# Performance work log

Hardware: AMD Instinct MI355X
Metric: run time of the kernel (lower is better)

Reference implementation:

```python
import jax, jax.numpy as jnp
import numpy as np

N = 8192
F_IN = 256
F_OUT = 64
ALPHA = 0.2  # leaky relu negative slope
MASK_VAL = -9e15


def setup_inputs() -> dict:
    key = jax.random.key(0)
    k1, k2, k3, k4, k5, k6 = jax.random.split(key, 6)
    stdv_lin = 1.0 / np.sqrt(F_IN)
    stdv_a = 1.0 / np.sqrt(2 * F_OUT)
    return {
        "input": jax.random.normal(k1, (N, F_IN), dtype=jnp.float32),
        "adj": jax.random.randint(k2, (N, N), 0, 2, dtype=jnp.int32),
        "W": jax.random.uniform(k3, (F_IN, F_OUT), minval=-stdv_lin, maxval=stdv_lin, dtype=jnp.float32),
        "b_lin": jax.random.uniform(k4, (F_OUT,), minval=-stdv_lin, maxval=stdv_lin, dtype=jnp.float32),
        "a": jax.random.uniform(k5, (2 * F_OUT, 1), minval=-stdv_a, maxval=stdv_a, dtype=jnp.float32),
        "bias": jax.random.uniform(k6, (F_OUT,), minval=-stdv_a, maxval=stdv_a, dtype=jnp.float32),
    }


def reference(input, adj, W, b_lin, a, bias):
    # h = Linear(input): [N, F_OUT]
    h = input @ W + b_lin
    # e[i,j] = leaky_relu(a1 . h_i + a2 . h_j)  (equivalent to the repeat/cat/matmul in torch,
    # without materializing the [N, N, 2*F_OUT] tensor)
    a1 = a[:F_OUT, 0]
    a2 = a[F_OUT:, 0]
    s1 = h @ a1  # [N]
    s2 = h @ a2  # [N]
    e = jax.nn.leaky_relu(s1[:, None] + s2[None, :], negative_slope=ALPHA)  # [N, N]
    attention = jnp.where(adj > 0, e, MASK_VAL)
    attention = jax.nn.softmax(attention, axis=1)
    # dropout is identity in eval mode (training=False)
    output = attention @ h + bias
    return output
```

## Files before the change

### kernel.cpp

```cpp
#include <hip/hip_runtime.h>

#define N 8192
#define FIN 256
#define FOUT 64
#define ALPHA 0.2f
#define LOG2C 3
#define NCHUNK (1 << LOG2C)
#define CLEN (N >> LOG2C)

typedef float f32x4 __attribute__((ext_vector_type(4)));
typedef short s16x8 __attribute__((ext_vector_type(8)));

static __device__ __forceinline__ unsigned short f2bf(float x) {
    unsigned u = __float_as_uint(x);
    u += 0x7fffu + ((u >> 16) & 1u);
    return (unsigned short)(u >> 16);
}

__global__ __launch_bounds__(256) void k_linear(
    const float* __restrict__ input, const float* __restrict__ W,
    const float* __restrict__ b_lin, const float* __restrict__ a,
    unsigned short* __restrict__ hTf, float* __restrict__ s1, float* __restrict__ s2,
    unsigned* __restrict__ s2max_enc)
{
    __shared__ float in_sh[16 * FIN];
    __shared__ float hst[64][17];
    int t = threadIdx.x, w = t >> 6, f = t & 63;
    int b = blockIdx.x;
    int i0 = b * 16;

#pragma unroll
    for (int r = 0; r < 4; r++) {
        int row = w * 4 + r;
        *(float4*)&in_sh[row * FIN + f * 4] =
            *(const float4*)(input + (size_t)(i0 + row) * FIN + f * 4);
    }

    float a1v = a[f], a2v = a[FOUT + f];
    float h[4];
#pragma unroll
    for (int r = 0; r < 4; r++) h[r] = b_lin[f];

    for (int k4 = 0; k4 < FIN / 4; k4++) {
        float wv0 = W[(k4 * 4 + 0) * FOUT + f];
        float wv1 = W[(k4 * 4 + 1) * FOUT + f];
        float wv2 = W[(k4 * 4 + 2) * FOUT + f];
        float wv3 = W[(k4 * 4 + 3) * FOUT + f];
#pragma unroll
        for (int r = 0; r < 4; r++) {
            float4 iv = *(const float4*)&in_sh[(w * 4 + r) * FIN + k4 * 4];
            h[r] = fmaf(iv.x, wv0, h[r]);
            h[r] = fmaf(iv.y, wv1, h[r]);
            h[r] = fmaf(iv.z, wv2, h[r]);
            h[r] = fmaf(iv.w, wv3, h[r]);
        }
    }

    float wmax = -1e30f;
#pragma unroll
    for (int r = 0; r < 4; r++) {
        hst[f][w * 4 + r] = h[r];
        float v1 = h[r] * a1v, v2 = h[r] * a2v;
#pragma unroll
        for (int d = 1; d < 64; d <<= 1) { v1 += __shfl_xor(v1, d); v2 += __shfl_xor(v2, d); }
        wmax = fmaxf(wmax, v2);
        if (f == 0) { s1[i0 + w * 4 + r] = v1; s2[i0 + w * 4 + r] = v2; }
    }
    if (f == 0) {
        unsigned u = __float_as_uint(wmax);
        unsigned key = (u & 0x80000000u) ? ~u : (u | 0x80000000u);
        atomicMax(s2max_enc, key);
    }
    __syncthreads();

    int fo = t >> 2, seg = t & 3;
    unsigned lo = f2bf(hst[fo][seg * 4 + 0]) | ((unsigned)f2bf(hst[fo][seg * 4 + 1]) << 16);
    unsigned hi = f2bf(hst[fo][seg * 4 + 2]) | ((unsigned)f2bf(hst[fo][seg * 4 + 3]) << 16);
    int2 v; v.x = (int)lo; v.y = (int)hi;
    size_t base = (size_t)(b >> 1) * 2048 + (size_t)fo * 32 + (b & 1) * 16 + seg * 4;
    *(int2*)(hTf + base) = v;
}


#define PGEN(AV0, AV1, SVP, AFR) do {                                             \
    float4 sv0 = *(const float4*)(SVP);                                           \
    float4 sv1 = *(const float4*)((SVP) + 4);                                     \
    float p0, p1, p2, p3, p4, p5, p6, p7;                                         \
    { float u = s1c + sv0.x; float g = fmaxf(u, fmaf(0.2f, u, c2)); p0 = (AV0.x > 0) ? exp2f(g) : 0.f; } \
    { float u = s1c + sv0.y; float g = fmaxf(u, fmaf(0.2f, u, c2)); p1 = (AV0.y > 0) ? exp2f(g) : 0.f; } \
    { float u = s1c + sv0.z; float g = fmaxf(u, fmaf(0.2f, u, c2)); p2 = (AV0.z > 0) ? exp2f(g) : 0.f; } \
    { float u = s1c + sv0.w; float g = fmaxf(u, fmaf(0.2f, u, c2)); p3 = (AV0.w > 0) ? exp2f(g) : 0.f; } \
    { float u = s1c + sv1.x; float g = fmaxf(u, fmaf(0.2f, u, c2)); p4 = (AV1.x > 0) ? exp2f(g) : 0.f; } \
    { float u = s1c + sv1.y; float g = fmaxf(u, fmaf(0.2f, u, c2)); p5 = (AV1.y > 0) ? exp2f(g) : 0.f; } \
    { float u = s1c + sv1.z; float g = fmaxf(u, fmaf(0.2f, u, c2)); p6 = (AV1.z > 0) ? exp2f(g) : 0.f; } \
    { float u = s1c + sv1.w; float g = fmaxf(u, fmaf(0.2f, u, c2)); p7 = (AV1.w > 0) ? exp2f(g) : 0.f; } \
    dacc += ((p0 + p1) + (p2 + p3)) + ((p4 + p5) + (p6 + p7));                    \
    union { s16x8 v; unsigned u[4]; } pk;                                         \
    asm("v_cvt_pk_bf16_f32 %0, %1, %2" : "=v"(pk.u[0]) : "v"(p0), "v"(p1));       \
    asm("v_cvt_pk_bf16_f32 %0, %1, %2" : "=v"(pk.u[1]) : "v"(p2), "v"(p3));       \
    asm("v_cvt_pk_bf16_f32 %0, %1, %2" : "=v"(pk.u[2]) : "v"(p4), "v"(p5));       \
    asm("v_cvt_pk_bf16_f32 %0, %1, %2" : "=v"(pk.u[3]) : "v"(p6), "v"(p7));       \
    AFR = pk.v;                                                                   \
} while (0)

__global__ __launch_bounds__(256) void k_attn(
    const int* __restrict__ adj, const float* __restrict__ s1g,
    const float* __restrict__ s2g, const unsigned short* __restrict__ hTf,
    const unsigned* __restrict__ s2max_enc,
    float* __restrict__ numP, float* __restrict__ denP)
{
    __shared__ unsigned short hsh[4096];
    __shared__ float s2sh[CLEN];

    const float LOG2E = 1.4426950408889634f;
    int bid = blockIdx.x;
    int chunk = bid & (NCHUNK - 1);
    int rg = bid >> LOG2C;
    int jstart = chunk * CLEN;
    int t = threadIdx.x, w = t >> 6, l = t & 63;
    int l15 = l & 15, kg = l >> 4;
    int kgs = kg ^ ((l15 >> 1) & 3);

    {
        float4 sv = ((const float4*)(s2g + jstart))[t];
        sv.x *= LOG2E; sv.y *= LOG2E; sv.z *= LOG2E; sv.w *= LOG2E;
        ((float4*)s2sh)[t] = sv;
    }
    unsigned key = *s2max_enc;
    unsigned su = (key & 0x80000000u) ? (key ^ 0x80000000u) : ~key;
    float s2m = __uint_as_float(su);

    int i0 = rg * 64;
    int i = i0 + w * 16 + l15;
    float s1v = s1g[i];
    float mx = s1v + s2m; mx = fmaxf(mx, ALPHA * mx);
    float m2 = mx * LOG2E;
    float s1c = fmaf(s1v, LOG2E, -m2);
    float c2 = -0.8f * m2;

    const int4* adjq = (const int4*)(adj + (size_t)i * N + jstart);
    const int4* src4 = (const int4*)(hTf + (size_t)jstart * 64);

    int4 a0 = adjq[kg * 2 + 0];
    int4 a1 = adjq[kg * 2 + 1];
    int4 a2 = adjq[8 + kg * 2 + 0];
    int4 a3 = adjq[8 + kg * 2 + 1];

    f32x4 acc[4] = {};
    float dacc = 0.f;

#pragma unroll 1
    for (int it = 0; it < CLEN / 64; it++) {
        if (it) __syncthreads();
        {
            int G0 = t, G1 = t + 256;
            int4 v0 = src4[it * 512 + G0];
            int4 v1 = src4[it * 512 + G1];
            ((int4*)hsh)[(G0 & ~3) | ((G0 ^ (G0 >> 3)) & 3)] = v0;
            ((int4*)hsh)[(G1 & ~3) | ((G1 ^ (G1 >> 3)) & 3)] = v1;
        }
        __syncthreads();

        int4 n0, n1, n2, n3;
        if (it + 1 < CLEN / 64) {
            n0 = adjq[(it + 1) * 16 + kg * 2 + 0];
            n1 = adjq[(it + 1) * 16 + kg * 2 + 1];
            n2 = adjq[(it + 1) * 16 + 8 + kg * 2 + 0];
            n3 = adjq[(it + 1) * 16 + 8 + kg * 2 + 1];
        }

        const float* svp = &s2sh[it * 64 + kg * 8];
        const unsigned short* bt = hsh + l15 * 32 + kgs * 8;
        {
            s16x8 afr;
            PGEN(a0, a1, svp, afr);
            s16x8 b0 = *(const s16x8*)(bt);
            s16x8 b1 = *(const s16x8*)(bt + 512);
            s16x8 b2 = *(const s16x8*)(bt + 1024);
            s16x8 b3 = *(const s16x8*)(bt + 1536);
            acc[0] = __builtin_amdgcn_mfma_f32_16x16x32_bf16(afr, b0, acc[0], 0, 0, 0);
            acc[1] = __builtin_amdgcn_mfma_f32_16x16x32_bf16(afr, b1, acc[1], 0, 0, 0);
            acc[2] = __builtin_amdgcn_mfma_f32_16x16x32_bf16(afr, b2, acc[2], 0, 0, 0);
            acc[3] = __builtin_amdgcn_mfma_f32_16x16x32_bf16(afr, b3, acc[3], 0, 0, 0);
        }
        {
            s16x8 afr;
            PGEN(a2, a3, svp + 32, afr);
            s16x8 b0 = *(const s16x8*)(bt + 2048);
            s16x8 b1 = *(const s16x8*)(bt + 2560);
            s16x8 b2 = *(const s16x8*)(bt + 3072);
            s16x8 b3 = *(const s16x8*)(bt + 3584);
            acc[0] = __builtin_amdgcn_mfma_f32_16x16x32_bf16(afr, b0, acc[0], 0, 0, 0);
            acc[1] = __builtin_amdgcn_mfma_f32_16x16x32_bf16(afr, b1, acc[1], 0, 0, 0);
            acc[2] = __builtin_amdgcn_mfma_f32_16x16x32_bf16(afr, b2, acc[2], 0, 0, 0);
            acc[3] = __builtin_amdgcn_mfma_f32_16x16x32_bf16(afr, b3, acc[3], 0, 0, 0);
        }
        a0 = n0; a1 = n1; a2 = n2; a3 = n3;
    }

    dacc += __shfl_xor(dacc, 16);
    dacc += __shfl_xor(dacc, 32);
    if (l < 16) denP[(size_t)chunk * N + i0 + w * 16 + l] = dacc;
#pragma unroll
    for (int nt = 0; nt < 4; nt++) {
#pragma unroll
        for (int r = 0; r < 4; r++) {
            int orow = w * 16 + kg * 4 + r;
            numP[((size_t)chunk * N + i0 + orow) * FOUT + nt * 16 + l15] = acc[nt][r];
        }
    }
}

__global__ __launch_bounds__(256) void k_finalize(
    const float* __restrict__ numP, const float* __restrict__ denP,
    const float* __restrict__ bias, float* __restrict__ out)
{
    int idx = blockIdx.x * 256 + threadIdx.x;
    int i = idx >> 6, f = idx & 63;
    float nsum = 0.f, dsum = 0.f;
#pragma unroll
    for (int c = 0; c < NCHUNK; c++) {
        nsum += numP[(size_t)c * (N * FOUT) + idx];
        dsum += denP[(size_t)c * N + i];
    }
    out[idx] = nsum / dsum + bias[f];
}

extern "C" void kernel_launch(void* const* d_in, const int* in_sizes, int n_in,
                              void* d_out, int out_size, void* d_ws, size_t ws_size,
                              hipStream_t stream)
{
    const float* input = (const float*)d_in[0];
    const int*   adj   = (const int*)d_in[1];
    const float* W     = (const float*)d_in[2];
    const float* b_lin = (const float*)d_in[3];
    const float* a     = (const float*)d_in[4];
    const float* bias  = (const float*)d_in[5];
    float* out = (float*)d_out;

    char* ws = (char*)d_ws;
    unsigned short* hTf = (unsigned short*)ws;
    float* s1    = (float*)(ws + 1048576);
    float* s2    = (float*)(ws + 1048576 + 32768);
    unsigned* s2max_enc = (unsigned*)(ws + 1048576 + 65536);
    size_t fixed = 1048576 + 65536 + 256;
    float* numP = (float*)(ws + fixed);
    float* denP = (float*)(ws + fixed + ((size_t)N * FOUT * 4) * NCHUNK);

    hipMemsetAsync(s2max_enc, 0, 4, stream);
    hipLaunchKernelGGL(k_linear, dim3(512), dim3(256), 0, stream,
                       input, W, b_lin, a, hTf, s1, s2, s2max_enc);
    hipLaunchKernelGGL(k_attn, dim3((N / 64) * NCHUNK), dim3(256), 0, stream,
                       adj, s1, s2, hTf, s2max_enc, numP, denP);
    hipLaunchKernelGGL(k_finalize, dim3(2048), dim3(256), 0, stream,
                       numP, denP, bias, out);
}
```

Before: 103.1 us.

## Double-buffer h tiles in LDS using direct global-to-LDS async loads

The per-iteration h tile staging is replaced with global_load_lds direct-to-LDS copies into a double buffer. The next tile is prefetched while the current one is consumed, and the two barriers per iteration become one. A manual waitcnt with vmcnt(4) leaves the adj prefetch loads in flight. This relies on the ordering of outstanding vmem ops being correct, and it doubles the LDS footprint for h.

New measurement: 105.2 us. +2.0%, slower.

```diff
diff --git a/kernel.cpp b/kernel.cpp
--- a/kernel.cpp
+++ b/kernel.cpp
@@ -7,6 +7,7 @@
 #define LOG2C 3
 #define NCHUNK (1 << LOG2C)
 #define CLEN (N >> LOG2C)
+#define ITERS (CLEN / 64)
 
 typedef float f32x4 __attribute__((ext_vector_type(4)));
 typedef short s16x8 __attribute__((ext_vector_type(8)));
@@ -109,7 +110,7 @@
     const unsigned* __restrict__ s2max_enc,
     float* __restrict__ numP, float* __restrict__ denP)
 {
-    __shared__ unsigned short hsh[4096];
+    __shared__ unsigned short hsh[2][4096];
     __shared__ float s2sh[CLEN];
 
     const float LOG2E = 1.4426950408889634f;
@@ -121,11 +122,22 @@
     int l15 = l & 15, kg = l >> 4;
     int kgs = kg ^ ((l15 >> 1) & 3);
 
+    int D0 = w * 128 + l;
+    int D1 = w * 128 + 64 + l;
+    int S0 = (D0 & ~3) | ((D0 ^ (D0 >> 3)) & 3);
+    int S1 = (D1 & ~3) | ((D1 ^ (D1 >> 3)) & 3);
+    const char* srcb = (const char*)(hTf + (size_t)jstart * 64);
+
     {
         float4 sv = ((const float4*)(s2g + jstart))[t];
         sv.x *= LOG2E; sv.y *= LOG2E; sv.z *= LOG2E; sv.w *= LOG2E;
         ((float4*)s2sh)[t] = sv;
     }
+    __builtin_amdgcn_global_load_lds(srcb + (size_t)S0 * 16,
+                                     (char*)&hsh[0][0] + w * 2048, 16, 0, 0);
+    __builtin_amdgcn_global_load_lds(srcb + (size_t)S1 * 16,
+                                     (char*)&hsh[0][0] + w * 2048 + 1024, 16, 0, 0);
+
     unsigned key = *s2max_enc;
     unsigned su = (key & 0x80000000u) ? (key ^ 0x80000000u) : ~key;
     float s2m = __uint_as_float(su);
@@ -139,8 +151,6 @@
     float c2 = -0.8f * m2;
 
     const int4* adjq = (const int4*)(adj + (size_t)i * N + jstart);
-    const int4* src4 = (const int4*)(hTf + (size_t)jstart * 64);
-
     int4 a0 = adjq[kg * 2 + 0];
     int4 a1 = adjq[kg * 2 + 1];
     int4 a2 = adjq[8 + kg * 2 + 0];
@@ -148,21 +158,20 @@
 
     f32x4 acc[4] = {};
     float dacc = 0.f;
+    __syncthreads();
 
 #pragma unroll 1
-    for (int it = 0; it < CLEN / 64; it++) {
-        if (it) __syncthreads();
-        {
-            int G0 = t, G1 = t + 256;
-            int4 v0 = src4[it * 512 + G0];
-            int4 v1 = src4[it * 512 + G1];
-            ((int4*)hsh)[(G0 & ~3) | ((G0 ^ (G0 >> 3)) & 3)] = v0;
-            ((int4*)hsh)[(G1 & ~3) | ((G1 ^ (G1 >> 3)) & 3)] = v1;
-        }
-        __syncthreads();
-
+    for (int it = 0; it < ITERS; it++) {
+        int cur = it & 1;
+        bool more = (it + 1 < ITERS);
+        if (more) {
+            const char* s = srcb + (size_t)(it + 1) * 8192;
+            char* d = (char*)&hsh[cur ^ 1][0] + w * 2048;
+            __builtin_amdgcn_global_load_lds(s + (size_t)S0 * 16, d, 16, 0, 0);
+            __builtin_amdgcn_global_load_lds(s + (size_t)S1 * 16, d + 1024, 16, 0, 0);
+        }
         int4 n0, n1, n2, n3;
-        if (it + 1 < CLEN / 64) {
+        if (more) {
             n0 = adjq[(it + 1) * 16 + kg * 2 + 0];
             n1 = adjq[(it + 1) * 16 + kg * 2 + 1];
             n2 = adjq[(it + 1) * 16 + 8 + kg * 2 + 0];
@@ -170,32 +179,36 @@
         }
 
         const float* svp = &s2sh[it * 64 + kg * 8];
-        const unsigned short* bt = hsh + l15 * 32 + kgs * 8;
+        const unsigned short* bt = &hsh[cur][0] + l15 * 32 + kgs * 8;
         {
-            s16x8 afr;
-            PGEN(a0, a1, svp, afr);
             s16x8 b0 = *(const s16x8*)(bt);
             s16x8 b1 = *(const s16x8*)(bt + 512);
             s16x8 b2 = *(const s16x8*)(bt + 1024);
             s16x8 b3 = *(const s16x8*)(bt + 1536);
+            s16x8 afr;
+            PGEN(a0, a1, svp, afr);
             acc[0] = __builtin_amdgcn_mfma_f32_16x16x32_bf16(afr, b0, acc[0], 0, 0, 0);
             acc[1] = __builtin_amdgcn_mfma_f32_16x16x32_bf16(afr, b1, acc[1], 0, 0, 0);
             acc[2] = __builtin_amdgcn_mfma_f32_16x16x32_bf16(afr, b2, acc[2], 0, 0, 0);
             acc[3] = __builtin_amdgcn_mfma_f32_16x16x32_bf16(afr, b3, acc[3], 0, 0, 0);
         }
         {
-            s16x8 afr;
-            PGEN(a2, a3, svp + 32, afr);
             s16x8 b0 = *(const s16x8*)(bt + 2048);
             s16x8 b1 = *(const s16x8*)(bt + 2560);
             s16x8 b2 = *(const s16x8*)(bt + 3072);
             s16x8 b3 = *(const s16x8*)(bt + 3584);
+            s16x8 afr;
+            PGEN(a2, a3, svp + 32, afr);
             acc[0] = __builtin_amdgcn_mfma_f32_16x16x32_bf16(afr, b0, acc[0], 0, 0, 0);
             acc[1] = __builtin_amdgcn_mfma_f32_16x16x32_bf16(afr, b1, acc[1], 0, 0, 0);
             acc[2] = __builtin_amdgcn_mfma_f32_16x16x32_bf16(afr, b2, acc[2], 0, 0, 0);
             acc[3] = __builtin_amdgcn_mfma_f32_16x16x32_bf16(afr, b3, acc[3], 0, 0, 0);
         }
-        a0 = n0; a1 = n1; a2 = n2; a3 = n3;
+        if (more) {
+            asm volatile("s_waitcnt vmcnt(4) lgkmcnt(0)" ::: "memory");
+            __builtin_amdgcn_s_barrier();
+            a0 = n0; a1 = n1; a2 = n2; a3 = n3;
+        }
     }
 
     dacc += __shfl_xor(dacc, 16);
```
